# Kernel tuning notes

Measured on AMD Instinct MI355X. Metric: run time of the kernel, lower is better.

Reference implementation:

```python
import jax, jax.numpy as jnp
import numpy as np

N = 100000
E = 1600000
D = 128
H = 128


def gcn_conv(x, W, b, src, dst, n_nodes):
    # x: [N, Din] -> linear transform first (PyG GCNConv)
    h = x @ W  # [N, Dout]
    # add self loops
    loop = jnp.arange(n_nodes, dtype=src.dtype)
    s = jnp.concatenate([src, loop])
    d = jnp.concatenate([dst, loop])
    # symmetric normalization: deg computed on destination (col) with unit weights
    deg = jnp.zeros((n_nodes,), dtype=h.dtype).at[d].add(1.0)
    dinv = jnp.where(deg > 0, jax.lax.rsqrt(deg), 0.0)
    norm = dinv[s] * dinv[d]  # [E+N]
    msg = h[s] * norm[:, None]  # gather + scale
    out = jax.ops.segment_sum(msg, d, num_segments=n_nodes)
    return out + b


def setup_inputs() -> dict:
    key = jax.random.key(0)
    ks = jax.random.split(key, 8)
    x = jax.random.normal(ks[0], (N, D), dtype=jnp.float32)
    edge_index = jax.random.randint(ks[1], (2, E), 0, N, dtype=jnp.int32)
    sc = 1.0 / np.sqrt(D)
    gate_W = jax.random.uniform(ks[2], (D, D), jnp.float32, -sc, sc)
    gate_b = jax.random.uniform(ks[3], (D,), jnp.float32, -sc, sc)
    W1 = jax.random.normal(ks[4], (D, H), dtype=jnp.float32) * sc
    b1 = jnp.zeros((H,), jnp.float32)
    W2 = jax.random.normal(ks[5], (H, H), dtype=jnp.float32) * (1.0 / np.sqrt(H))
    b2 = jnp.zeros((H,), jnp.float32)
    return {"x": x, "edge_index": edge_index, "gate_W": gate_W, "gate_b": gate_b,
            "W1": W1, "b1": b1, "W2": W2, "b2": b2}


def reference(x, edge_index, gate_W, gate_b, W1, b1, W2, b2):
    src, dst = edge_index[0], edge_index[1]
    gate = jax.nn.sigmoid(x @ gate_W + gate_b)
    h = x * gate
    h = gcn_conv(h, W1, b1, src, dst, N)
    h = jax.nn.relu(h)
    h = gcn_conv(h, W2, b2, src, dst, N)
    return h
```

## Files before the change

### kernel.cpp

```cpp
#include <hip/hip_runtime.h>
#include <hip/hip_bf16.h>
#include <math.h>


#define BUCKET_SHIFT 8
#define BUCKET_W 256
#define CAP 4864
#define NB_MAX 512
#define OSTRIDE 136

typedef __attribute__((ext_vector_type(8))) short bf16x8;
typedef __attribute__((ext_vector_type(4))) float f32x4;

__device__ __forceinline__ unsigned short f2bf(float x) {
    unsigned int u = __float_as_uint(x);
    unsigned int r = (u + 0x7FFFu + ((u >> 16) & 1u)) >> 16;
    return (unsigned short)r;
}
__device__ __forceinline__ float blo(unsigned int u) { return __uint_as_float(u << 16); }
__device__ __forceinline__ float bhi(unsigned int u) { return __uint_as_float(u & 0xFFFF0000u); }

__device__ __forceinline__ void cvt_hilo8(const float* v, bf16x8& hi, bf16x8& lo) {
#pragma unroll
    for (int j = 0; j < 8; j++) {
        unsigned short h = f2bf(v[j]);
        float hf = __uint_as_float((unsigned int)h << 16);
        hi[j] = (short)h;
        lo[j] = (short)f2bf(v[j] - hf);
    }
}

__device__ __forceinline__ f32x4 MF(bf16x8 a, bf16x8 b, f32x4 c) {
    return __builtin_amdgcn_mfma_f32_16x16x32_bf16(a, b, c, 0, 0, 0);
}

__global__ __launch_bounds__(512)
void prepinit_kernel(const float* __restrict__ W0, const float* __restrict__ W1,
                     const float* __restrict__ W2, uint4* __restrict__ img,
                     int* __restrict__ bcursor, int NB) {
    int b = blockIdx.x, t = threadIdx.x;
    if (b < 12) {
        int idx = b * 512 + t;
        int c = idx & 127, kb = (idx >> 7) & 15, w = idx >> 11;
        const float* W = (w == 0) ? W0 : (w == 1) ? W1 : W2;
        bf16x8 hb;
#pragma unroll
        for (int j = 0; j < 8; j++) hb[j] = (short)f2bf(W[(size_t)(kb * 8 + j) * 128 + c]);
        img[w * 2048 + c * 16 + (kb ^ (c & 15))] = *(uint4*)&hb;
    } else {
        if (t < NB) bcursor[t] = 0;
    }
}

__device__ __forceinline__ void partition_body(char* smem, int b, int t,
                                               const int* __restrict__ src,
                                               const int* __restrict__ dst,
                                               int* __restrict__ bucketCursor,
                                               unsigned int* __restrict__ part,
                                               int E, int NB, int chunk) {
    int* hist  = (int*)smem;
    int* basec = hist + NB_MAX;
    int e0 = b * chunk;
    int e1 = min(E, e0 + chunk);

    for (int i = t; i < NB; i += 512) hist[i] = 0;
    __syncthreads();
    for (int e = e0 + t; e < e1; e += 512) {
        int bb = dst[e] >> BUCKET_SHIFT;
        atomicAdd(&hist[bb], 1);
    }
    __syncthreads();
    for (int i = t; i < NB; i += 512) {
        int c = hist[i];
        basec[i] = c ? atomicAdd(&bucketCursor[i], c) : 0;
    }
    __syncthreads();
    for (int i = t; i < NB; i += 512) hist[i] = 0;
    __syncthreads();
    for (int e = e0 + t; e < e1; e += 512) {
        int d = dst[e], s = src[e];
        int bb = d >> BUCKET_SHIFT;
        int r = atomicAdd(&hist[bb], 1);
        int pos = basec[bb] + r;
        if (pos < CAP)
            part[(size_t)bb * CAP + pos] = ((unsigned int)(d & (BUCKET_W - 1)) << 17) | (unsigned int)s;
    }
}

__device__ __forceinline__ void gate_body(char* smem, int gb, int t,
                                          const float* __restrict__ x,
                                          const uint4* __restrict__ gimg,
                                          const float* __restrict__ gate_b,
                                          unsigned short* __restrict__ hpack, int n) {
    uint4* Wl = (uint4*)smem;
    unsigned short* OutS = (unsigned short*)(smem + 32768);
    int lane = t & 63, wv = t >> 6;
    int blockRow = gb * 128;

    for (int idx = t; idx < 2048; idx += 512) Wl[idx] = gimg[idx];

    bf16x8 Ahi[4], Alo[4];
    {
        int arow = blockRow + wv * 16 + (lane & 15);
        const float* ap = x + (size_t)min(arow, n - 1) * 128 + (lane >> 4) * 8;
#pragma unroll
        for (int s = 0; s < 4; s++) {
            float v[8];
            *(float4*)&v[0] = *(const float4*)&ap[s * 32];
            *(float4*)&v[4] = *(const float4*)&ap[s * 32 + 4];
            cvt_hilo8(v, Ahi[s], Alo[s]);
        }
    }
    __syncthreads();

    f32x4 acc[8];
#pragma unroll
    for (int nt = 0; nt < 8; nt++) acc[nt] = (f32x4)(0.f);
#pragma unroll
    for (int s = 0; s < 4; s++) {
        int kb = s * 4 + (lane >> 4);
#pragma unroll
        for (int nt = 0; nt < 8; nt++) {
            int c = nt * 16 + (lane & 15);
            bf16x8 bh = *(bf16x8*)&Wl[c * 16 + (kb ^ (lane & 15))];
            acc[nt] = MF(Ahi[s], bh, acc[nt]);
            acc[nt] = MF(Alo[s], bh, acc[nt]);
        }
    }

    int rl0 = wv * 16 + (lane >> 4) * 4;
#pragma unroll
    for (int nt = 0; nt < 8; nt++) {
        int c = nt * 16 + (lane & 15);
        float gb2 = gate_b[c];
#pragma unroll
        for (int r = 0; r < 4; r++) {
            int grow = min(blockRow + rl0 + r, n - 1);
            float xv = x[(size_t)grow * 128 + c];
            float hv = xv / (1.f + __expf(-(acc[nt][r] + gb2)));
            OutS[(rl0 + r) * OSTRIDE + c] = f2bf(hv);
        }
    }
    __syncthreads();
    {
        int row = t >> 2;
        int c0 = (t & 3) * 32;
        int grow = blockRow + row;
        if (grow < n) {
#pragma unroll
            for (int j = 0; j < 4; j++) {
                uint4 v = *(uint4*)&OutS[row * OSTRIDE + c0 + j * 8];
                *(uint4*)&hpack[(size_t)grow * 128 + c0 + j * 8] = v;
            }
        }
    }
}

__global__ __launch_bounds__(512)
void pg_kernel(const int* __restrict__ src, const int* __restrict__ dst,
               int* __restrict__ bucketCursor, unsigned int* __restrict__ part,
               int E, int NB, int chunk,
               const float* __restrict__ x, const uint4* __restrict__ gimg,
               const float* __restrict__ gate_b, unsigned short* __restrict__ hpack, int n) {
    __shared__ __align__(16) char smem[67584];
    int b = blockIdx.x, t = threadIdx.x;
    if (b < 256) partition_body(smem, b, t, src, dst, bucketCursor, part, E, NB, chunk);
    else         gate_body(smem, b - 256, t, x, gimg, gate_b, hpack, n);
}

__global__ __launch_bounds__(512)
void bucket_scan_kernel(const int* __restrict__ bucketCursor,
                        int* __restrict__ bucketBase, int NB) {
    __shared__ int sm[NB_MAX];
    int t = threadIdx.x;
    int v = (t < NB) ? min(bucketCursor[t], CAP) : 0;
    sm[t] = v;
    __syncthreads();
    for (int off = 1; off < NB_MAX; off <<= 1) {
        int a = (t >= off) ? sm[t - off] : 0;
        __syncthreads();
        sm[t] += a;
        __syncthreads();
    }
    if (t < NB) bucketBase[t + 1] = sm[t];
    if (t == 0) bucketBase[0] = 0;
}

__device__ __forceinline__ void fill_body(char* smem, int b, int t,
                                          const unsigned int* __restrict__ part,
                                          const int* __restrict__ bucketBase,
                                          int* __restrict__ rowptr, float* __restrict__ dinv,
                                          int* __restrict__ col, int N, int NB) {
    unsigned int* eLDS = (unsigned int*)smem;
    int* deg  = (int*)(smem + CAP * 4);
    int* cur  = deg + BUCKET_W;
    int* wsum = cur + BUCKET_W;

    int base = bucketBase[b];
    int cnt = bucketBase[b + 1] - base;

    for (int i = t; i < cnt; i += 512) eLDS[i] = part[(size_t)b * CAP + i];
    if (t < 256) deg[t] = 0;
    __syncthreads();
    for (int i = t; i < cnt; i += 512) atomicAdd(&deg[eLDS[i] >> 17], 1);
    __syncthreads();

    int v = (t < 256) ? deg[t] : 0;
    int incl = v;
    int lane = t & 63, w = t >> 6;
    for (int off = 1; off < 64; off <<= 1) {
        int u = __shfl_up(incl, off, 64);
        if (lane >= off) incl += u;
    }
    if (lane == 63) wsum[w] = incl;
    __syncthreads();
    int add = 0;
#pragma unroll
    for (int j = 0; j < 4; j++) if (j < w) add += wsum[j];
    int excl = add + incl - v;
    if (t < 256) {
        cur[t] = excl;
        int gnode = b * BUCKET_W + t;
        if (gnode < N) {
            rowptr[gnode] = base + excl;
            dinv[gnode] = rsqrtf((float)(v + 1));
        }
    }
    if (b == NB - 1 && t == 0) rowptr[N] = base + cnt;
    __syncthreads();

    for (int i = t; i < cnt; i += 512) {
        unsigned int ev = eLDS[i];
        int dl = ev >> 17;
        int p = atomicAdd(&cur[dl], 1);
        col[base + p] = (int)(ev & 0x1FFFFu);
    }
}

template <int SCALE>
__device__ __forceinline__ void gemm_body(char* smem, int gb, int t,
                                          const unsigned short* __restrict__ A,
                                          const uint4* __restrict__ wimg,
                                          const float* __restrict__ dinv,
                                          unsigned short* __restrict__ g, int n) {
    uint4* Wl = (uint4*)smem;
    unsigned short* OutS = (unsigned short*)(smem + 32768);
    int lane = t & 63, wv = t >> 6;
    int blockRow = gb * 128;

    for (int idx = t; idx < 2048; idx += 512) Wl[idx] = wimg[idx];

    bf16x8 Af[4];
    {
        int arow = blockRow + wv * 16 + (lane & 15);
        const uint4* ap = (const uint4*)(A + (size_t)min(arow, n - 1) * 128);
#pragma unroll
        for (int s = 0; s < 4; s++) {
            uint4 u = ap[(lane >> 4) + s * 4];
            Af[s] = *(bf16x8*)&u;
        }
    }
    __syncthreads();

    f32x4 acc[8];
#pragma unroll
    for (int nt = 0; nt < 8; nt++) acc[nt] = (f32x4)(0.f);
#pragma unroll
    for (int s = 0; s < 4; s++) {
        int kb = s * 4 + (lane >> 4);
#pragma unroll
        for (int nt = 0; nt < 8; nt++) {
            int c = nt * 16 + (lane & 15);
            bf16x8 bh = *(bf16x8*)&Wl[c * 16 + (kb ^ (lane & 15))];
            acc[nt] = MF(Af[s], bh, acc[nt]);
        }
    }

    int rl0 = wv * 16 + (lane >> 4) * 4;
    float di[4];
#pragma unroll
    for (int r = 0; r < 4; r++)
        di[r] = SCALE ? dinv[min(blockRow + rl0 + r, n - 1)] : 1.f;
#pragma unroll
    for (int nt = 0; nt < 8; nt++) {
        int c = nt * 16 + (lane & 15);
#pragma unroll
        for (int r = 0; r < 4; r++)
            OutS[(rl0 + r) * OSTRIDE + c] = f2bf(acc[nt][r] * di[r]);
    }
    __syncthreads();
    {
        int row = t >> 2;
        int c0 = (t & 3) * 32;
        int grow = blockRow + row;
        if (grow < n) {
#pragma unroll
            for (int j = 0; j < 4; j++) {
                uint4 v = *(uint4*)&OutS[row * OSTRIDE + c0 + j * 8];
                *(uint4*)&g[(size_t)grow * 128 + c0 + j * 8] = v;
            }
        }
    }
}

__global__ __launch_bounds__(512)
void fg_kernel(const unsigned int* __restrict__ part, const int* __restrict__ bucketBase,
               int* __restrict__ rowptr, float* __restrict__ dinv, int* __restrict__ col,
               int N, int NB,
               const unsigned short* __restrict__ A, const uint4* __restrict__ wimg,
               unsigned short* __restrict__ g) {
    __shared__ __align__(16) char smem[67584];
    int b = blockIdx.x, t = threadIdx.x;
    if (b < NB) fill_body(smem, b, t, part, bucketBase, rowptr, dinv, col, N, NB);
    else        gemm_body<0>(smem, b - NB, t, A, wimg, (const float*)nullptr, g, N);
}

__global__ __launch_bounds__(512)
void gemm_bf16_kernel(const unsigned short* __restrict__ A, const uint4* __restrict__ wimg,
                      const float* __restrict__ dinv, unsigned short* __restrict__ g, int n) {
    __shared__ __align__(16) char smem[67584];
    gemm_body<1>(smem, blockIdx.x, threadIdx.x, A, wimg, dinv, g, n);
}

template <int RELU, int PACK, int DVSRC>
__global__ void spmm_kernel(const uint4* __restrict__ g16, const int* __restrict__ rowptr,
                            const int* __restrict__ col, const float* __restrict__ dinv,
                            const float* __restrict__ bias, void* __restrict__ outv,
                            int n, int nhb) {
    int half = (blockIdx.x >= nhb) ? 1 : 0;
    int rb = blockIdx.x - half * nhb;
    int i = rb * 32 + (threadIdx.x >> 3);
    if (i >= n) return;
    int c = threadIdx.x & 7;

    float di = dinv[i];
    const uint4* gp = g16 + half * 8 + c;
    float acc[8];
    uint4 sv = gp[(size_t)i * 16];
    float wi = DVSRC ? di : 1.f;
    acc[0] = wi * blo(sv.x); acc[1] = wi * bhi(sv.x);
    acc[2] = wi * blo(sv.y); acc[3] = wi * bhi(sv.y);
    acc[4] = wi * blo(sv.z); acc[5] = wi * bhi(sv.z);
    acc[6] = wi * blo(sv.w); acc[7] = wi * bhi(sv.w);

    int e0 = rowptr[i], e1 = rowptr[i + 1];
    int e = e0;
    for (; e + 4 <= e1; e += 4) {
        int s0 = col[e], s1 = col[e + 1], s2 = col[e + 2], s3 = col[e + 3];
        uint4 v0 = gp[(size_t)s0 * 16];
        uint4 v1 = gp[(size_t)s1 * 16];
        uint4 v2 = gp[(size_t)s2 * 16];
        uint4 v3 = gp[(size_t)s3 * 16];
        float w0 = DVSRC ? dinv[s0] : 1.f;
        float w1 = DVSRC ? dinv[s1] : 1.f;
        float w2 = DVSRC ? dinv[s2] : 1.f;
        float w3 = DVSRC ? dinv[s3] : 1.f;
        acc[0] = fmaf(w0, blo(v0.x), fmaf(w1, blo(v1.x), fmaf(w2, blo(v2.x), fmaf(w3, blo(v3.x), acc[0]))));
        acc[1] = fmaf(w0, bhi(v0.x), fmaf(w1, bhi(v1.x), fmaf(w2, bhi(v2.x), fmaf(w3, bhi(v3.x), acc[1]))));
        acc[2] = fmaf(w0, blo(v0.y), fmaf(w1, blo(v1.y), fmaf(w2, blo(v2.y), fmaf(w3, blo(v3.y), acc[2]))));
        acc[3] = fmaf(w0, bhi(v0.y), fmaf(w1, bhi(v1.y), fmaf(w2, bhi(v2.y), fmaf(w3, bhi(v3.y), acc[3]))));
        acc[4] = fmaf(w0, blo(v0.z), fmaf(w1, blo(v1.z), fmaf(w2, blo(v2.z), fmaf(w3, blo(v3.z), acc[4]))));
        acc[5] = fmaf(w0, bhi(v0.z), fmaf(w1, bhi(v1.z), fmaf(w2, bhi(v2.z), fmaf(w3, bhi(v3.z), acc[5]))));
        acc[6] = fmaf(w0, blo(v0.w), fmaf(w1, blo(v1.w), fmaf(w2, blo(v2.w), fmaf(w3, blo(v3.w), acc[6]))));
        acc[7] = fmaf(w0, bhi(v0.w), fmaf(w1, bhi(v1.w), fmaf(w2, bhi(v2.w), fmaf(w3, bhi(v3.w), acc[7]))));
    }
    for (; e < e1; e++) {
        int s0 = col[e];
        uint4 v0 = gp[(size_t)s0 * 16];
        float w0 = DVSRC ? dinv[s0] : 1.f;
        acc[0] = fmaf(w0, blo(v0.x), acc[0]); acc[1] = fmaf(w0, bhi(v0.x), acc[1]);
        acc[2] = fmaf(w0, blo(v0.y), acc[2]); acc[3] = fmaf(w0, bhi(v0.y), acc[3]);
        acc[4] = fmaf(w0, blo(v0.z), acc[4]); acc[5] = fmaf(w0, bhi(v0.z), acc[5]);
        acc[6] = fmaf(w0, blo(v0.w), acc[6]); acc[7] = fmaf(w0, bhi(v0.w), acc[7]);
    }

    const float4* b4 = (const float4*)(bias + half * 64);
    float4 bv0 = b4[c * 2], bv1 = b4[c * 2 + 1];
    float r0[8];
    r0[0] = fmaf(acc[0], di, bv0.x);
    r0[1] = fmaf(acc[1], di, bv0.y);
    r0[2] = fmaf(acc[2], di, bv0.z);
    r0[3] = fmaf(acc[3], di, bv0.w);
    r0[4] = fmaf(acc[4], di, bv1.x);
    r0[5] = fmaf(acc[5], di, bv1.y);
    r0[6] = fmaf(acc[6], di, bv1.z);
    r0[7] = fmaf(acc[7], di, bv1.w);
    if (RELU) {
#pragma unroll
        for (int j = 0; j < 8; j++) r0[j] = fmaxf(r0[j], 0.f);
    }
    if (PACK) {
        uint4 w;
        w.x = (unsigned int)f2bf(r0[0]) | ((unsigned int)f2bf(r0[1]) << 16);
        w.y = (unsigned int)f2bf(r0[2]) | ((unsigned int)f2bf(r0[3]) << 16);
        w.z = (unsigned int)f2bf(r0[4]) | ((unsigned int)f2bf(r0[5]) << 16);
        w.w = (unsigned int)f2bf(r0[6]) | ((unsigned int)f2bf(r0[7]) << 16);
        *(uint4*)((unsigned short*)outv + (size_t)i * 128 + half * 64 + c * 8) = w;
    } else {
        float* o = (float*)outv + (size_t)i * 128 + half * 64 + c * 8;
        f32x4 a = *(f32x4*)&r0[0];
        f32x4 b = *(f32x4*)&r0[4];
        __builtin_nontemporal_store(a, (f32x4*)o);
        __builtin_nontemporal_store(b, (f32x4*)(o + 4));
    }
}

extern "C" void kernel_launch(void* const* d_in, const int* in_sizes, int n_in,
                              void* d_out, int out_size, void* d_ws, size_t ws_size,
                              hipStream_t stream) {
    const float* x      = (const float*)d_in[0];
    const int*   ei     = (const int*)d_in[1];
    const float* gate_W = (const float*)d_in[2];
    const float* gate_b = (const float*)d_in[3];
    const float* W1     = (const float*)d_in[4];
    const float* b1     = (const float*)d_in[5];
    const float* W2     = (const float*)d_in[6];
    const float* b2     = (const float*)d_in[7];
    float* out = (float*)d_out;

    const int N = in_sizes[0] / 128;
    const int E = in_sizes[1] / 2;
    const int* src = ei;
    const int* dst = ei + E;
    const int NB = (N + BUCKET_W - 1) / BUCKET_W;

    char* p = (char*)d_ws;
    auto alloc = [&](size_t bytes) { char* q = p; p += (bytes + 255) & ~(size_t)255; return q; };
    int*   rowptr  = (int*)alloc(((size_t)N + 1) * 4);
    float* dinv    = (float*)alloc((size_t)N * 4);
    int*   colb    = (int*)alloc((size_t)E * 4);
    int*   bcursor = (int*)alloc((size_t)NB * 4);
    int*   bbase   = (int*)alloc(((size_t)NB + 1) * 4);
    uint4* wimg    = (uint4*)alloc((size_t)3 * 2048 * 16);
    unsigned int*   part   = (unsigned int*)alloc((size_t)NB * CAP * 4);
    unsigned short* hpack  = (unsigned short*)alloc((size_t)N * 128 * 2);
    unsigned short* g16    = (unsigned short*)alloc((size_t)N * 128 * 2);
    unsigned short* h1pack = (unsigned short*)alloc((size_t)N * 128 * 2);

    const int pblocks = 256;
    const int chunk = (E + pblocks - 1) / pblocks;
    int gblocks = (N + 127) / 128;
    int nhb = (N + 31) / 32;

    prepinit_kernel<<<13, 512, 0, stream>>>(gate_W, W1, W2, wimg, bcursor, NB);
    pg_kernel<<<256 + gblocks, 512, 0, stream>>>(src, dst, bcursor, part, E, NB, chunk,
                                                 x, wimg, gate_b, hpack, N);
    bucket_scan_kernel<<<1, 512, 0, stream>>>(bcursor, bbase, NB);
    fg_kernel<<<NB + gblocks, 512, 0, stream>>>(part, bbase, rowptr, dinv, colb, N, NB,
                                                hpack, wimg + 2048, g16);
    spmm_kernel<1, 1, 1><<<2 * nhb, 256, 0, stream>>>((const uint4*)g16, rowptr, colb,
                                                      dinv, b1, h1pack, N, nhb);
    gemm_bf16_kernel<<<gblocks, 512, 0, stream>>>(h1pack, wimg + 4096, dinv, g16, N);
    spmm_kernel<0, 0, 0><<<2 * nhb, 256, 0, stream>>>((const uint4*)g16, rowptr, colb,
                                                      dinv, b2, out, N, nhb);
}
```

Measured before the change: 215.6 us.

## Split SpMM feature dimension into quarters with interleaved block scheduling

The SpMM kernel now splits each 128-feature row into four 32-feature quarters, each handled by 4 lanes, and interleaves quarter and row-half indices in the low bits of the block index. Blocks running at the same time therefore gather different column slices from two row halves, which is meant to make each concurrent wave's gather working set smaller and more cache-resident. Blocks grow to 512 threads (128 rows each). The cost is that every edge index and dinv value is read four times instead of twice, and each gathered row segment is only 64 bytes.

Result: slower. 320.0 us (+48.4%).

```diff
diff --git a/kernel.cpp b/kernel.cpp
--- a/kernel.cpp
+++ b/kernel.cpp
@@ -323,18 +323,24 @@
 }
 
 template <int RELU, int PACK, int DVSRC>
-__global__ void spmm_kernel(const uint4* __restrict__ g16, const int* __restrict__ rowptr,
-                            const int* __restrict__ col, const float* __restrict__ dinv,
-                            const float* __restrict__ bias, void* __restrict__ outv,
-                            int n, int nhb) {
-    int half = (blockIdx.x >= nhb) ? 1 : 0;
-    int rb = blockIdx.x - half * nhb;
-    int i = rb * 32 + (threadIdx.x >> 3);
+__global__ __launch_bounds__(512)
+void spmm_kernel(const uint4* __restrict__ g16, const int* __restrict__ rowptr,
+                 const int* __restrict__ col, const float* __restrict__ dinv,
+                 const float* __restrict__ bias, void* __restrict__ outv,
+                 int n, int halfN) {
+    int combo = blockIdx.x & 7;
+    int rb = blockIdx.x >> 3;
+    int s = combo & 3;
+    int rh = combo >> 2;
+    int lr = rb * 128 + (threadIdx.x >> 2);
+    if (lr >= halfN) return;
+    int i = rh * halfN + lr;
     if (i >= n) return;
-    int c = threadIdx.x & 7;
+    int l4 = threadIdx.x & 3;
+    int qoff = s * 4 + l4;
 
     float di = dinv[i];
-    const uint4* gp = g16 + half * 8 + c;
+    const uint4* gp = g16 + qoff;
     float acc[8];
     uint4 sv = gp[(size_t)i * 16];
     float wi = DVSRC ? di : 1.f;
@@ -374,8 +380,9 @@
         acc[6] = fmaf(w0, blo(v0.w), acc[6]); acc[7] = fmaf(w0, bhi(v0.w), acc[7]);
     }
 
-    const float4* b4 = (const float4*)(bias + half * 64);
-    float4 bv0 = b4[c * 2], bv1 = b4[c * 2 + 1];
+    const float* bp = bias + s * 32 + l4 * 8;
+    float4 bv0 = *(const float4*)&bp[0];
+    float4 bv1 = *(const float4*)&bp[4];
     float r0[8];
     r0[0] = fmaf(acc[0], di, bv0.x);
     r0[1] = fmaf(acc[1], di, bv0.y);
@@ -395,9 +402,9 @@
         w.y = (unsigned int)f2bf(r0[2]) | ((unsigned int)f2bf(r0[3]) << 16);
         w.z = (unsigned int)f2bf(r0[4]) | ((unsigned int)f2bf(r0[5]) << 16);
         w.w = (unsigned int)f2bf(r0[6]) | ((unsigned int)f2bf(r0[7]) << 16);
-        *(uint4*)((unsigned short*)outv + (size_t)i * 128 + half * 64 + c * 8) = w;
+        *(uint4*)((unsigned short*)outv + (size_t)i * 128 + s * 32 + l4 * 8) = w;
     } else {
-        float* o = (float*)outv + (size_t)i * 128 + half * 64 + c * 8;
+        float* o = (float*)outv + (size_t)i * 128 + s * 32 + l4 * 8;
         f32x4 a = *(f32x4*)&r0[0];
         f32x4 b = *(f32x4*)&r0[4];
         __builtin_nontemporal_store(a, (f32x4*)o);
@@ -440,7 +447,8 @@
     const int pblocks = 256;
     const int chunk = (E + pblocks - 1) / pblocks;
     int gblocks = (N + 127) / 128;
-    int nhb = (N + 31) / 32;
+    int halfN = (N + 1) / 2;
+    int nrb = (halfN + 127) / 128;
 
     prepinit_kernel<<<13, 512, 0, stream>>>(gate_W, W1, W2, wimg, bcursor, NB);
     pg_kernel<<<256 + gblocks, 512, 0, stream>>>(src, dst, bcursor, part, E, NB, chunk,
@@ -448,9 +456,9 @@
     bucket_scan_kernel<<<1, 512, 0, stream>>>(bcursor, bbase, NB);
     fg_kernel<<<NB + gblocks, 512, 0, stream>>>(part, bbase, rowptr, dinv, colb, N, NB,
                                                 hpack, wimg + 2048, g16);
-    spmm_kernel<1, 1, 1><<<2 * nhb, 256, 0, stream>>>((const uint4*)g16, rowptr, colb,
-                                                      dinv, b1, h1pack, N, nhb);
+    spmm_kernel<1, 1, 1><<<8 * nrb, 512, 0, stream>>>((const uint4*)g16, rowptr, colb,
+                                                      dinv, b1, h1pack, N, halfN);
     gemm_bf16_kernel<<<gblocks, 512, 0, stream>>>(h1pack, wimg + 4096, dinv, g16, N);
-    spmm_kernel<0, 0, 0><<<2 * nhb, 256, 0, stream>>>((const uint4*)g16, rowptr, colb,
-                                                      dinv, b2, out, N, nhb);
-}
+    spmm_kernel<0, 0, 0><<<8 * nrb, 512, 0, stream>>>((const uint4*)g16, rowptr, colb,
+                                                      dinv, b2, out, N, halfN);
+}
```

## Fuse first-layer SpMM with second-layer GEMM via shared-memory tile

Applied to the files above, without the earlier changes.

Merges the layer-1 aggregation (gather, normalize, bias, ReLU) with the layer-2 dense transform in one kernel. Each 64-row block builds its post-ReLU tile in LDS and multiplies it by W2 there, so the intermediate activation no longer makes a round trip through global memory and one launch is dropped. The second SpMM now relies on rows already scaled by the source-side dinv, which turns its inner loop into plain adds with no per-edge dinv loads. In exchange, the fused kernel gathers full 256-byte rows per node with 8 threads, only 2 edges in flight per iteration, and a larger LDS footprint that may reduce occupancy.

Measured after the change: 212.2 us. About the same (-1.6%).

```diff
diff --git a/kernel.cpp b/kernel.cpp
--- a/kernel.cpp
+++ b/kernel.cpp
@@ -237,11 +237,9 @@
     }
 }
 
-template <int SCALE>
 __device__ __forceinline__ void gemm_body(char* smem, int gb, int t,
                                           const unsigned short* __restrict__ A,
                                           const uint4* __restrict__ wimg,
-                                          const float* __restrict__ dinv,
                                           unsigned short* __restrict__ g, int n) {
     uint4* Wl = (uint4*)smem;
     unsigned short* OutS = (unsigned short*)(smem + 32768);
@@ -277,16 +275,12 @@
     }
 
     int rl0 = wv * 16 + (lane >> 4) * 4;
-    float di[4];
-#pragma unroll
-    for (int r = 0; r < 4; r++)
-        di[r] = SCALE ? dinv[min(blockRow + rl0 + r, n - 1)] : 1.f;
 #pragma unroll
     for (int nt = 0; nt < 8; nt++) {
         int c = nt * 16 + (lane & 15);
 #pragma unroll
         for (int r = 0; r < 4; r++)
-            OutS[(rl0 + r) * OSTRIDE + c] = f2bf(acc[nt][r] * di[r]);
+            OutS[(rl0 + r) * OSTRIDE + c] = f2bf(acc[nt][r]);
     }
     __syncthreads();
     {
@@ -312,20 +306,175 @@
     __shared__ __align__(16) char smem[67584];
     int b = blockIdx.x, t = threadIdx.x;
     if (b < NB) fill_body(smem, b, t, part, bucketBase, rowptr, dinv, col, N, NB);
-    else        gemm_body<0>(smem, b - NB, t, A, wimg, (const float*)nullptr, g, N);
+    else        gemm_body(smem, b - NB, t, A, wimg, g, N);
 }
 
 __global__ __launch_bounds__(512)
-void gemm_bf16_kernel(const unsigned short* __restrict__ A, const uint4* __restrict__ wimg,
-                      const float* __restrict__ dinv, unsigned short* __restrict__ g, int n) {
-    __shared__ __align__(16) char smem[67584];
-    gemm_body<1>(smem, blockIdx.x, threadIdx.x, A, wimg, dinv, g, n);
-}
-
-template <int RELU, int PACK, int DVSRC>
+void spmm_gemm_kernel(const uint4* __restrict__ g16, const int* __restrict__ rowptr,
+                      const int* __restrict__ col, const float* __restrict__ dinv,
+                      const float* __restrict__ b1, const uint4* __restrict__ w2img,
+                      unsigned short* __restrict__ g2, int n) {
+    __shared__ __align__(16) char smem[49664];
+    uint4* W2l = (uint4*)smem;
+    uint4* Hl  = (uint4*)(smem + 32768);
+    float* dl  = (float*)(smem + 49152);
+    unsigned short* OutS = (unsigned short*)smem;
+
+    int t = threadIdx.x;
+    int blockRow = blockIdx.x * 64;
+
+    for (int idx = t; idx < 2048; idx += 512) W2l[idx] = w2img[idx];
+
+    int r = t >> 3, l = t & 7;
+    int i = min(blockRow + r, n - 1);
+    float di = dinv[i];
+    if (l == 0) dl[r] = di;
+
+    float acc[16];
+    {
+        uint4 s0 = g16[(size_t)i * 16 + l];
+        uint4 s1 = g16[(size_t)i * 16 + 8 + l];
+        acc[0] = di * blo(s0.x);  acc[1] = di * bhi(s0.x);
+        acc[2] = di * blo(s0.y);  acc[3] = di * bhi(s0.y);
+        acc[4] = di * blo(s0.z);  acc[5] = di * bhi(s0.z);
+        acc[6] = di * blo(s0.w);  acc[7] = di * bhi(s0.w);
+        acc[8] = di * blo(s1.x);  acc[9] = di * bhi(s1.x);
+        acc[10] = di * blo(s1.y); acc[11] = di * bhi(s1.y);
+        acc[12] = di * blo(s1.z); acc[13] = di * bhi(s1.z);
+        acc[14] = di * blo(s1.w); acc[15] = di * bhi(s1.w);
+    }
+    int e0 = rowptr[i], e1 = rowptr[i + 1];
+    int e = e0;
+    for (; e + 2 <= e1; e += 2) {
+        int s0 = col[e], s1 = col[e + 1];
+        uint4 a0 = g16[(size_t)s0 * 16 + l];
+        uint4 a1 = g16[(size_t)s0 * 16 + 8 + l];
+        uint4 c0 = g16[(size_t)s1 * 16 + l];
+        uint4 c1 = g16[(size_t)s1 * 16 + 8 + l];
+        float w0 = dinv[s0], w1 = dinv[s1];
+        acc[0]  = fmaf(w0, blo(a0.x), fmaf(w1, blo(c0.x), acc[0]));
+        acc[1]  = fmaf(w0, bhi(a0.x), fmaf(w1, bhi(c0.x), acc[1]));
+        acc[2]  = fmaf(w0, blo(a0.y), fmaf(w1, blo(c0.y), acc[2]));
+        acc[3]  = fmaf(w0, bhi(a0.y), fmaf(w1, bhi(c0.y), acc[3]));
+        acc[4]  = fmaf(w0, blo(a0.z), fmaf(w1, blo(c0.z), acc[4]));
+        acc[5]  = fmaf(w0, bhi(a0.z), fmaf(w1, bhi(c0.z), acc[5]));
+        acc[6]  = fmaf(w0, blo(a0.w), fmaf(w1, blo(c0.w), acc[6]));
+        acc[7]  = fmaf(w0, bhi(a0.w), fmaf(w1, bhi(c0.w), acc[7]));
+        acc[8]  = fmaf(w0, blo(a1.x), fmaf(w1, blo(c1.x), acc[8]));
+        acc[9]  = fmaf(w0, bhi(a1.x), fmaf(w1, bhi(c1.x), acc[9]));
+        acc[10] = fmaf(w0, blo(a1.y), fmaf(w1, blo(c1.y), acc[10]));
+        acc[11] = fmaf(w0, bhi(a1.y), fmaf(w1, bhi(c1.y), acc[11]));
+        acc[12] = fmaf(w0, blo(a1.z), fmaf(w1, blo(c1.z), acc[12]));
+        acc[13] = fmaf(w0, bhi(a1.z), fmaf(w1, bhi(c1.z), acc[13]));
+        acc[14] = fmaf(w0, blo(a1.w), fmaf(w1, blo(c1.w), acc[14]));
+        acc[15] = fmaf(w0, bhi(a1.w), fmaf(w1, bhi(c1.w), acc[15]));
+    }
+    if (e < e1) {
+        int s0 = col[e];
+        uint4 a0 = g16[(size_t)s0 * 16 + l];
+        uint4 a1 = g16[(size_t)s0 * 16 + 8 + l];
+        float w0 = dinv[s0];
+        acc[0]  = fmaf(w0, blo(a0.x), acc[0]);  acc[1]  = fmaf(w0, bhi(a0.x), acc[1]);
+        acc[2]  = fmaf(w0, blo(a0.y), acc[2]);  acc[3]  = fmaf(w0, bhi(a0.y), acc[3]);
+        acc[4]  = fmaf(w0, blo(a0.z), acc[4]);  acc[5]  = fmaf(w0, bhi(a0.z), acc[5]);
+        acc[6]  = fmaf(w0, blo(a0.w), acc[6]);  acc[7]  = fmaf(w0, bhi(a0.w), acc[7]);
+        acc[8]  = fmaf(w0, blo(a1.x), acc[8]);  acc[9]  = fmaf(w0, bhi(a1.x), acc[9]);
+        acc[10] = fmaf(w0, blo(a1.y), acc[10]); acc[11] = fmaf(w0, bhi(a1.y), acc[11]);
+        acc[12] = fmaf(w0, blo(a1.z), acc[12]); acc[13] = fmaf(w0, bhi(a1.z), acc[13]);
+        acc[14] = fmaf(w0, blo(a1.w), acc[14]); acc[15] = fmaf(w0, bhi(a1.w), acc[15]);
+    }
+
+    {
+        const float* bp0 = b1 + l * 8;
+        const float* bp1 = b1 + 64 + l * 8;
+        float4 b00 = *(const float4*)&bp0[0], b01 = *(const float4*)&bp0[4];
+        float4 b10 = *(const float4*)&bp1[0], b11 = *(const float4*)&bp1[4];
+        float h[16];
+        h[0] = fmaxf(fmaf(acc[0], di, b00.x), 0.f);
+        h[1] = fmaxf(fmaf(acc[1], di, b00.y), 0.f);
+        h[2] = fmaxf(fmaf(acc[2], di, b00.z), 0.f);
+        h[3] = fmaxf(fmaf(acc[3], di, b00.w), 0.f);
+        h[4] = fmaxf(fmaf(acc[4], di, b01.x), 0.f);
+        h[5] = fmaxf(fmaf(acc[5], di, b01.y), 0.f);
+        h[6] = fmaxf(fmaf(acc[6], di, b01.z), 0.f);
+        h[7] = fmaxf(fmaf(acc[7], di, b01.w), 0.f);
+        h[8] = fmaxf(fmaf(acc[8], di, b10.x), 0.f);
+        h[9] = fmaxf(fmaf(acc[9], di, b10.y), 0.f);
+        h[10] = fmaxf(fmaf(acc[10], di, b10.z), 0.f);
+        h[11] = fmaxf(fmaf(acc[11], di, b10.w), 0.f);
+        h[12] = fmaxf(fmaf(acc[12], di, b11.x), 0.f);
+        h[13] = fmaxf(fmaf(acc[13], di, b11.y), 0.f);
+        h[14] = fmaxf(fmaf(acc[14], di, b11.z), 0.f);
+        h[15] = fmaxf(fmaf(acc[15], di, b11.w), 0.f);
+        uint4 p0, p1;
+        p0.x = (unsigned int)f2bf(h[0]) | ((unsigned int)f2bf(h[1]) << 16);
+        p0.y = (unsigned int)f2bf(h[2]) | ((unsigned int)f2bf(h[3]) << 16);
+        p0.z = (unsigned int)f2bf(h[4]) | ((unsigned int)f2bf(h[5]) << 16);
+        p0.w = (unsigned int)f2bf(h[6]) | ((unsigned int)f2bf(h[7]) << 16);
+        p1.x = (unsigned int)f2bf(h[8]) | ((unsigned int)f2bf(h[9]) << 16);
+        p1.y = (unsigned int)f2bf(h[10]) | ((unsigned int)f2bf(h[11]) << 16);
+        p1.z = (unsigned int)f2bf(h[12]) | ((unsigned int)f2bf(h[13]) << 16);
+        p1.w = (unsigned int)f2bf(h[14]) | ((unsigned int)f2bf(h[15]) << 16);
+        int sw = r & 15;
+        Hl[r * 16 + (l ^ sw)] = p0;
+        Hl[r * 16 + ((l + 8) ^ sw)] = p1;
+    }
+    __syncthreads();
+
+    int lane = t & 63, wv = t >> 6;
+    int rt = wv & 3, ch = wv >> 2;
+    bf16x8 Af[4];
+    {
+        int arow = rt * 16 + (lane & 15);
+        int asw = arow & 15;
+#pragma unroll
+        for (int s = 0; s < 4; s++) {
+            int kb = s * 4 + (lane >> 4);
+            uint4 u = Hl[arow * 16 + (kb ^ asw)];
+            Af[s] = *(bf16x8*)&u;
+        }
+    }
+    f32x4 acc2[4];
+#pragma unroll
+    for (int ntl = 0; ntl < 4; ntl++) acc2[ntl] = (f32x4)(0.f);
+#pragma unroll
+    for (int s = 0; s < 4; s++) {
+        int kb = s * 4 + (lane >> 4);
+#pragma unroll
+        for (int ntl = 0; ntl < 4; ntl++) {
+            int c = (ch * 4 + ntl) * 16 + (lane & 15);
+            bf16x8 bh = *(bf16x8*)&W2l[c * 16 + (kb ^ (lane & 15))];
+            acc2[ntl] = MF(Af[s], bh, acc2[ntl]);
+        }
+    }
+
+    int rl0 = rt * 16 + (lane >> 4) * 4;
+    float dr[4];
+#pragma unroll
+    for (int rr = 0; rr < 4; rr++) dr[rr] = dl[rl0 + rr];
+    __syncthreads();
+#pragma unroll
+    for (int ntl = 0; ntl < 4; ntl++) {
+        int c = (ch * 4 + ntl) * 16 + (lane & 15);
+#pragma unroll
+        for (int rr = 0; rr < 4; rr++)
+            OutS[(rl0 + rr) * OSTRIDE + c] = f2bf(acc2[ntl][rr] * dr[rr]);
+    }
+    __syncthreads();
+    {
+        int grow = blockRow + r;
+        if (grow < n) {
+            uint4 v0 = *(uint4*)&OutS[r * OSTRIDE + l * 16];
+            uint4 v1 = *(uint4*)&OutS[r * OSTRIDE + l * 16 + 8];
+            *(uint4*)&g2[(size_t)grow * 128 + l * 16] = v0;
+            *(uint4*)&g2[(size_t)grow * 128 + l * 16 + 8] = v1;
+        }
+    }
+}
+
 __global__ void spmm_kernel(const uint4* __restrict__ g16, const int* __restrict__ rowptr,
                             const int* __restrict__ col, const float* __restrict__ dinv,
-                            const float* __restrict__ bias, void* __restrict__ outv,
+                            const float* __restrict__ bias, float* __restrict__ outv,
                             int n, int nhb) {
     int half = (blockIdx.x >= nhb) ? 1 : 0;
     int rb = blockIdx.x - half * nhb;
@@ -333,15 +482,13 @@
     if (i >= n) return;
     int c = threadIdx.x & 7;
 
-    float di = dinv[i];
     const uint4* gp = g16 + half * 8 + c;
     float acc[8];
     uint4 sv = gp[(size_t)i * 16];
-    float wi = DVSRC ? di : 1.f;
-    acc[0] = wi * blo(sv.x); acc[1] = wi * bhi(sv.x);
-    acc[2] = wi * blo(sv.y); acc[3] = wi * bhi(sv.y);
-    acc[4] = wi * blo(sv.z); acc[5] = wi * bhi(sv.z);
-    acc[6] = wi * blo(sv.w); acc[7] = wi * bhi(sv.w);
+    acc[0] = blo(sv.x); acc[1] = bhi(sv.x);
+    acc[2] = blo(sv.y); acc[3] = bhi(sv.y);
+    acc[4] = blo(sv.z); acc[5] = bhi(sv.z);
+    acc[6] = blo(sv.w); acc[7] = bhi(sv.w);
 
     int e0 = rowptr[i], e1 = rowptr[i + 1];
     int e = e0;
@@ -351,29 +498,25 @@
         uint4 v1 = gp[(size_t)s1 * 16];
         uint4 v2 = gp[(size_t)s2 * 16];
         uint4 v3 = gp[(size_t)s3 * 16];
-        float w0 = DVSRC ? dinv[s0] : 1.f;
-        float w1 = DVSRC ? dinv[s1] : 1.f;
-        float w2 = DVSRC ? dinv[s2] : 1.f;
-        float w3 = DVSRC ? dinv[s3] : 1.f;
-        acc[0] = fmaf(w0, blo(v0.x), fmaf(w1, blo(v1.x), fmaf(w2, blo(v2.x), fmaf(w3, blo(v3.x), acc[0]))));
-        acc[1] = fmaf(w0, bhi(v0.x), fmaf(w1, bhi(v1.x), fmaf(w2, bhi(v2.x), fmaf(w3, bhi(v3.x), acc[1]))));
-        acc[2] = fmaf(w0, blo(v0.y), fmaf(w1, blo(v1.y), fmaf(w2, blo(v2.y), fmaf(w3, blo(v3.y), acc[2]))));
-        acc[3] = fmaf(w0, bhi(v0.y), fmaf(w1, bhi(v1.y), fmaf(w2, bhi(v2.y), fmaf(w3, bhi(v3.y), acc[3]))));
-        acc[4] = fmaf(w0, blo(v0.z), fmaf(w1, blo(v1.z), fmaf(w2, blo(v2.z), fmaf(w3, blo(v3.z), acc[4]))));
-        acc[5] = fmaf(w0, bhi(v0.z), fmaf(w1, bhi(v1.z), fmaf(w2, bhi(v2.z), fmaf(w3, bhi(v3.z), acc[5]))));
-        acc[6] = fmaf(w0, blo(v0.w), fmaf(w1, blo(v1.w), fmaf(w2, blo(v2.w), fmaf(w3, blo(v3.w), acc[6]))));
-        acc[7] = fmaf(w0, bhi(v0.w), fmaf(w1, bhi(v1.w), fmaf(w2, bhi(v2.w), fmaf(w3, bhi(v3.w), acc[7]))));
+        acc[0] += (blo(v0.x) + blo(v1.x)) + (blo(v2.x) + blo(v3.x));
+        acc[1] += (bhi(v0.x) + bhi(v1.x)) + (bhi(v2.x) + bhi(v3.x));
+        acc[2] += (blo(v0.y) + blo(v1.y)) + (blo(v2.y) + blo(v3.y));
+        acc[3] += (bhi(v0.y) + bhi(v1.y)) + (bhi(v2.y) + bhi(v3.y));
+        acc[4] += (blo(v0.z) + blo(v1.z)) + (blo(v2.z) + blo(v3.z));
+        acc[5] += (bhi(v0.z) + bhi(v1.z)) + (bhi(v2.z) + bhi(v3.z));
+        acc[6] += (blo(v0.w) + blo(v1.w)) + (blo(v2.w) + blo(v3.w));
+        acc[7] += (bhi(v0.w) + bhi(v1.w)) + (bhi(v2.w) + bhi(v3.w));
     }
     for (; e < e1; e++) {
         int s0 = col[e];
         uint4 v0 = gp[(size_t)s0 * 16];
-        float w0 = DVSRC ? dinv[s0] : 1.f;
-        acc[0] = fmaf(w0, blo(v0.x), acc[0]); acc[1] = fmaf(w0, bhi(v0.x), acc[1]);
-        acc[2] = fmaf(w0, blo(v0.y), acc[2]); acc[3] = fmaf(w0, bhi(v0.y), acc[3]);
-        acc[4] = fmaf(w0, blo(v0.z), acc[4]); acc[5] = fmaf(w0, bhi(v0.z), acc[5]);
-        acc[6] = fmaf(w0, blo(v0.w), acc[6]); acc[7] = fmaf(w0, bhi(v0.w), acc[7]);
-    }
-
+        acc[0] += blo(v0.x); acc[1] += bhi(v0.x);
+        acc[2] += blo(v0.y); acc[3] += bhi(v0.y);
+        acc[4] += blo(v0.z); acc[5] += bhi(v0.z);
+        acc[6] += blo(v0.w); acc[7] += bhi(v0.w);
+    }
+
+    float di = dinv[i];
     const float4* b4 = (const float4*)(bias + half * 64);
     float4 bv0 = b4[c * 2], bv1 = b4[c * 2 + 1];
     float r0[8];
@@ -385,24 +528,11 @@
     r0[5] = fmaf(acc[5], di, bv1.y);
     r0[6] = fmaf(acc[6], di, bv1.z);
     r0[7] = fmaf(acc[7], di, bv1.w);
-    if (RELU) {
-#pragma unroll
-        for (int j = 0; j < 8; j++) r0[j] = fmaxf(r0[j], 0.f);
-    }
-    if (PACK) {
-        uint4 w;
-        w.x = (unsigned int)f2bf(r0[0]) | ((unsigned int)f2bf(r0[1]) << 16);
-        w.y = (unsigned int)f2bf(r0[2]) | ((unsigned int)f2bf(r0[3]) << 16);
-        w.z = (unsigned int)f2bf(r0[4]) | ((unsigned int)f2bf(r0[5]) << 16);
-        w.w = (unsigned int)f2bf(r0[6]) | ((unsigned int)f2bf(r0[7]) << 16);
-        *(uint4*)((unsigned short*)outv + (size_t)i * 128 + half * 64 + c * 8) = w;
-    } else {
-        float* o = (float*)outv + (size_t)i * 128 + half * 64 + c * 8;
-        f32x4 a = *(f32x4*)&r0[0];
-        f32x4 b = *(f32x4*)&r0[4];
-        __builtin_nontemporal_store(a, (f32x4*)o);
-        __builtin_nontemporal_store(b, (f32x4*)(o + 4));
-    }
+    float* o = outv + (size_t)i * 128 + half * 64 + c * 8;
+    f32x4 a = *(f32x4*)&r0[0];
+    f32x4 b = *(f32x4*)&r0[4];
+    __builtin_nontemporal_store(a, (f32x4*)o);
+    __builtin_nontemporal_store(b, (f32x4*)(o + 4));
 }
 
 extern "C" void kernel_launch(void* const* d_in, const int* in_sizes, int n_in,
@@ -435,11 +565,12 @@
     unsigned int*   part   = (unsigned int*)alloc((size_t)NB * CAP * 4);
     unsigned short* hpack  = (unsigned short*)alloc((size_t)N * 128 * 2);
     unsigned short* g16    = (unsigned short*)alloc((size_t)N * 128 * 2);
-    unsigned short* h1pack = (unsigned short*)alloc((size_t)N * 128 * 2);
+    unsigned short* g2buf  = (unsigned short*)alloc((size_t)N * 128 * 2);
 
     const int pblocks = 256;
     const int chunk = (E + pblocks - 1) / pblocks;
     int gblocks = (N + 127) / 128;
+    int fblocks = (N + 63) / 64;
     int nhb = (N + 31) / 32;
 
     prepinit_kernel<<<13, 512, 0, stream>>>(gate_W, W1, W2, wimg, bcursor, NB);
@@ -448,9 +579,8 @@
     bucket_scan_kernel<<<1, 512, 0, stream>>>(bcursor, bbase, NB);
     fg_kernel<<<NB + gblocks, 512, 0, stream>>>(part, bbase, rowptr, dinv, colb, N, NB,
                                                 hpack, wimg + 2048, g16);
-    spmm_kernel<1, 1, 1><<<2 * nhb, 256, 0, stream>>>((const uint4*)g16, rowptr, colb,
-                                                      dinv, b1, h1pack, N, nhb);
-    gemm_bf16_kernel<<<gblocks, 512, 0, stream>>>(h1pack, wimg + 4096, dinv, g16, N);
-    spmm_kernel<0, 0, 0><<<2 * nhb, 256, 0, stream>>>((const uint4*)g16, rowptr, colb,
-                                                      dinv, b2, out, N, nhb);
-}
+    spmm_gemm_kernel<<<fblocks, 512, 0, stream>>>((const uint4*)g16, rowptr, colb,
+                                                  dinv, b1, wimg + 4096, g2buf, N);
+    spmm_kernel<<<2 * nhb, 256, 0, stream>>>((const uint4*)g2buf, rowptr, colb,
+                                             dinv, b2, out, N, nhb);
+}
```
